# Kernel optimization log

Measured on AMD Instinct MI355X. Metric: run time of the kernel, lower is better.

Reference implementation:

```python
import jax, jax.numpy as jnp
import numpy as np

B, N, DIM = 4, 4096, 1024
HEADS, DIM_HEAD = 16, 64
HD = HEADS * DIM_HEAD  # 1024
SCALE = DIM_HEAD ** -0.5


def setup_inputs() -> dict:
    key = jax.random.key(0)
    k0, k1, k2 = jax.random.split(key, 3)
    x = jax.random.normal(k0, (B, N, DIM), dtype=jnp.float32)
    # nn.Linear(dim, 3*hd): weight stored transposed here as (dim, 3*hd) for x @ W
    Wqkv = jax.random.normal(k1, (DIM, 3 * HD), dtype=jnp.float32) * 0.02
    bqkv = jnp.zeros((3 * HD,), dtype=jnp.float32)
    Wout = jax.random.normal(k2, (HD, DIM), dtype=jnp.float32) * 0.02
    bout = jnp.zeros((DIM,), dtype=jnp.float32)
    return {"x": x, "Wqkv": Wqkv, "bqkv": bqkv, "Wout": Wout, "bout": bout}


def reference(x, Wqkv, bqkv, Wout, bout):
    b, n, _ = x.shape
    # qkv: (b, n, 3*hd) -> (b, n, 3, hd)
    qkv = (x @ Wqkv + bqkv).reshape(b, n, 3, HD)
    # permute(2,0,3,1) in torch: q,k,v each have shape (b, hd, n)
    # (NOTE: heads are NOT split out in the original module; attention runs over
    #  the feature axis. We reproduce that math exactly.)
    q = jnp.swapaxes(qkv[:, :, 0, :], 1, 2)  # (b, hd, n)
    k = jnp.swapaxes(qkv[:, :, 1, :], 1, 2)
    v = jnp.swapaxes(qkv[:, :, 2, :], 1, 2)
    # dots: (b, hd, hd)
    dots = jnp.einsum('bfn,bgn->bfg', q, k) * SCALE
    attn = jax.nn.softmax(dots, axis=-1)
    # out: (b, hd, n), then row-major reinterpret to (b, n, hd) as torch reshape does
    out = jnp.einsum('bfg,bgn->bfn', attn, v).reshape(b, n, HD)
    return out @ Wout + bout
```

## Files before the change

### kernel.cpp

```cpp
#include <hip/hip_runtime.h>
#include <hip/hip_bf16.h>

typedef _Float16 f16x8 __attribute__((ext_vector_type(8)));
typedef float f32x4 __attribute__((ext_vector_type(4)));
typedef unsigned short u16x4 __attribute__((ext_vector_type(4)));
typedef unsigned short u16x8 __attribute__((ext_vector_type(8)));

__device__ __forceinline__ unsigned short f2h(float f) {
    _Float16 h = (_Float16)f;
    union { _Float16 h; unsigned short u; } v; v.h = h;
    return v.u;
}

__device__ __forceinline__ void gload16(const void* g, void* s) {
    __builtin_amdgcn_global_load_lds((const __attribute__((address_space(1))) void*)g,
                                     (__attribute__((address_space(3))) void*)s, 16, 0, 0);
}

__global__ __launch_bounds__(256)
void zero_f32(float* __restrict__ p, int n4) {
    int i = blockIdx.x * 256 + threadIdx.x, st = gridDim.x * 256;
    for (; i < n4; i += st)
        reinterpret_cast<float4*>(p)[i] = make_float4(0.f, 0.f, 0.f, 0.f);
}

__global__ __launch_bounds__(256)
void cvt_f32_f16(const float* __restrict__ in, unsigned short* __restrict__ out, int n8) {
    int i = blockIdx.x * 256 + threadIdx.x, st = gridDim.x * 256;
    for (; i < n8; i += st) {
        float4 v0 = reinterpret_cast<const float4*>(in)[2 * i];
        float4 v1 = reinterpret_cast<const float4*>(in)[2 * i + 1];
        float a[8] = {v0.x, v0.y, v0.z, v0.w, v1.x, v1.y, v1.z, v1.w};
        u16x8 h;
        #pragma unroll
        for (int j = 0; j < 8; ++j) h[j] = f2h(a[j]);
        reinterpret_cast<u16x8*>(out)[i] = h;
    }
}

__global__ __launch_bounds__(256)
void transpose_cvt(const float* __restrict__ in, unsigned short* __restrict__ ot,
                   int R, int C) {
    __shared__ float T[64][65];
    const int r0 = blockIdx.y * 64, c0 = blockIdx.x * 64;
    const int t = threadIdx.x;
    const int lr = t >> 2, lcq = (t & 3) * 16;
    #pragma unroll
    for (int q = 0; q < 4; ++q) {
        float4 v = *reinterpret_cast<const float4*>(&in[(long long)(r0 + lr) * C + c0 + lcq + q * 4]);
        T[lr][lcq + q * 4 + 0] = v.x; T[lr][lcq + q * 4 + 1] = v.y;
        T[lr][lcq + q * 4 + 2] = v.z; T[lr][lcq + q * 4 + 3] = v.w;
    }
    __syncthreads();
    const int oc = t >> 2, orq = (t & 3) * 16;
    #pragma unroll
    for (int q = 0; q < 4; ++q) {
        u16x4 hv;
        #pragma unroll
        for (int j = 0; j < 4; ++j) hv[j] = f2h(T[orq + q * 4 + j][oc]);
        long long o = (long long)(c0 + oc) * R + r0 + orq + q * 4;
        *reinterpret_cast<u16x4*>(&ot[o]) = hv;
    }
}

template<int EPI>
__global__ __launch_bounds__(256)
void gemm_f16(const unsigned short* __restrict__ A, const unsigned short* __restrict__ B,
              int sk_shift, int ks_size,
              long long lda, long long ldb,
              long long sA, long long sB, long long sC,
              float* __restrict__ Cf, unsigned short* __restrict__ Ch, long long ldc,
              const float* __restrict__ bias, float scale,
              unsigned short* __restrict__ qt, unsigned short* __restrict__ kt,
              unsigned short* __restrict__ vout)
{
    __shared__ __align__(16) unsigned short SMEM[2][2][128][32];

    const int tid  = threadIdx.x;
    const int wave = tid >> 6, lane = tid & 63;
    const int m0 = blockIdx.y * 128, n0 = blockIdx.x * 128;
    const int bz = (int)(blockIdx.z >> sk_shift);
    const int ks = (int)(blockIdx.z & ((1u << sk_shift) - 1));
    const int kbeg = ks * ks_size, kend = kbeg + ks_size;
    const int wm = (wave >> 1) * 64, wn = (wave & 1) * 64;
    const int fr = lane & 15, kslot = lane >> 4;
    const int srow = lane >> 2;

    const unsigned short* Ag = A + sA * bz + (long long)m0 * lda;
    const unsigned short* Bg = B + sB * bz + (long long)n0 * ldb;
    char* const sBase0 = (char*)&SMEM[0][0][0][0];
    char* const sBase1 = (char*)&SMEM[1][0][0][0];

    f32x4 acc[4][4] = {};

    auto STAGE = [&](char* base, int k0) {
        #pragma unroll
        for (int i = 0; i < 2; ++i) {
            const int r = i * 64 + wave * 16 + srow;
            const int qsrc = ((lane & 3) ^ ((r >> 1) & 3)) * 8;
            gload16(Ag + (long long)r * lda + k0 + qsrc, base + i * 4096 + wave * 1024);
            gload16(Bg + (long long)r * ldb + k0 + qsrc, base + 8192 + i * 4096 + wave * 1024);
        }
    };

    STAGE(sBase0, kbeg);
    __syncthreads();

    int cur = 0;
    for (int k0 = kbeg; k0 < kend; k0 += 32) {
        char* const rd = cur ? sBase1 : sBase0;
        char* const wr = cur ? sBase0 : sBase1;
        if (k0 + 32 < kend) STAGE(wr, k0 + 32);

        f16x8 af[4], bf[4];
        #pragma unroll
        for (int t = 0; t < 4; ++t) {
            const int ra = wm + t * 16 + fr;
            const int rb = wn + t * 16 + fr;
            af[t] = *reinterpret_cast<const f16x8*>(rd + ra * 64 + ((kslot ^ ((ra >> 1) & 3)) << 4));
            bf[t] = *reinterpret_cast<const f16x8*>(rd + 8192 + rb * 64 + ((kslot ^ ((rb >> 1) & 3)) << 4));
        }
        __builtin_amdgcn_s_setprio(1);
        #pragma unroll
        for (int mi = 0; mi < 4; ++mi)
            #pragma unroll
            for (int ni = 0; ni < 4; ++ni)
                acc[mi][ni] = __builtin_amdgcn_mfma_f32_16x16x32_f16(af[mi], bf[ni], acc[mi][ni], 0, 0, 0);
        __builtin_amdgcn_s_setprio(0);
        __syncthreads();
        cur ^= 1;
    }

    unsigned short (*LT)[72] = reinterpret_cast<unsigned short(*)[72]>(sBase0 + wave * 2304);

    const int rb4 = (lane >> 4) * 4;

    if (EPI == 1 || EPI == 4) {
        #pragma unroll
        for (int mi = 0; mi < 4; ++mi) {
            const int rloc = wm + mi * 16 + rb4;
            #pragma unroll
            for (int ni = 0; ni < 4; ++ni) {
                const int c = n0 + wn + ni * 16 + fr;
                const float bv = (EPI == 1) ? bias[c] : 0.0f;
                long long base = sC * bz + (long long)(m0 + rloc) * ldc + c;
                #pragma unroll
                for (int rr = 0; rr < 4; ++rr) {
                    float v = acc[mi][ni][rr] * scale + bv;
                    if (EPI == 1) Cf[base + (long long)rr * ldc] = v;
                    else          atomicAdd(&Cf[base + (long long)rr * ldc], v);
                }
            }
        }
    } else if (EPI == 2) {
        #pragma unroll
        for (int mi = 0; mi < 4; ++mi) {
            #pragma unroll
            for (int ni = 0; ni < 4; ++ni)
                #pragma unroll
                for (int rr = 0; rr < 4; ++rr)
                    LT[rb4 + rr][ni * 16 + fr] = f2h(acc[mi][ni][rr] * scale);
            #pragma unroll
            for (int q = 0; q < 2; ++q) {
                const int r_l = q * 8 + (lane >> 3);
                const int f0  = (lane & 7) * 8;
                u16x8 hv = *reinterpret_cast<const u16x8*>(&LT[r_l][f0]);
                long long base = sC * bz + (long long)(m0 + wm + mi * 16 + r_l) * ldc + (n0 + wn) + f0;
                *reinterpret_cast<u16x8*>(&Ch[base]) = hv;
            }
        }
    } else {
        const int segw = (n0 + wn) >> 10;
        const int tokb = m0 + wm;
        const int bloc = tokb >> 12;
        const int nbb  = tokb & 4095;
        if (segw < 2) {
            unsigned short* pt = (segw == 0) ? qt : kt;
            #pragma unroll
            for (int ni = 0; ni < 4; ++ni) {
                const float bv = bias[n0 + wn + ni * 16 + fr];
                #pragma unroll
                for (int mi = 0; mi < 4; ++mi) {
                    u16x4 hv;
                    #pragma unroll
                    for (int rr = 0; rr < 4; ++rr)
                        hv[rr] = f2h(acc[mi][ni][rr] * scale + bv);
                    *reinterpret_cast<u16x4*>(&LT[fr][mi * 16 + rb4]) = hv;
                }
                #pragma unroll
                for (int q = 0; q < 4; ++q) {
                    const int f_l = q * 4 + (lane >> 4);
                    const int t0  = (lane & 15) * 4;
                    u16x4 hv = *reinterpret_cast<const u16x4*>(&LT[f_l][t0]);
                    const int lc = (n0 + wn + ni * 16 + f_l) & 1023;
                    *reinterpret_cast<u16x4*>(&pt[(long long)bloc * 4194304 +
                        (long long)lc * 4096 + nbb + t0]) = hv;
                }
            }
        } else {
            const int lc0 = (n0 + wn) & 1023;
            #pragma unroll
            for (int mi = 0; mi < 4; ++mi) {
                #pragma unroll
                for (int ni = 0; ni < 4; ++ni) {
                    const float bv = bias[n0 + wn + ni * 16 + fr];
                    #pragma unroll
                    for (int rr = 0; rr < 4; ++rr)
                        LT[rb4 + rr][ni * 16 + fr] = f2h(acc[mi][ni][rr] * scale + bv);
                }
                #pragma unroll
                for (int q = 0; q < 2; ++q) {
                    const int r_l = q * 8 + (lane >> 3);
                    const int f0  = (lane & 7) * 8;
                    u16x8 hv = *reinterpret_cast<const u16x8*>(&LT[r_l][f0]);
                    const int tok = nbb + mi * 16 + r_l;
                    *reinterpret_cast<u16x8*>(&vout[(long long)bloc * 4194304 +
                        (long long)tok * 1024 + lc0 + f0]) = hv;
                }
            }
        }
    }
}

__global__ __launch_bounds__(256)
void softmax_rows_1024(const float* __restrict__ in, unsigned short* __restrict__ out)
{
    const int tid = threadIdx.x;
    const int wave = tid >> 6, lane = tid & 63;
    const long long rowoff = (long long)blockIdx.x * 1024;
    float4 v = reinterpret_cast<const float4*>(in + rowoff)[tid];

    float mx = fmaxf(fmaxf(v.x, v.y), fmaxf(v.z, v.w));
    #pragma unroll
    for (int o = 32; o > 0; o >>= 1) mx = fmaxf(mx, __shfl_xor(mx, o));
    __shared__ float rmax[4];
    if (lane == 0) rmax[wave] = mx;
    __syncthreads();
    mx = fmaxf(fmaxf(rmax[0], rmax[1]), fmaxf(rmax[2], rmax[3]));

    float e0 = expf(v.x - mx), e1 = expf(v.y - mx), e2 = expf(v.z - mx), e3 = expf(v.w - mx);
    float s = e0 + e1 + e2 + e3;
    #pragma unroll
    for (int o = 32; o > 0; o >>= 1) s += __shfl_xor(s, o);
    __shared__ float rsum[4];
    if (lane == 0) rsum[wave] = s;
    __syncthreads();
    s = rsum[0] + rsum[1] + rsum[2] + rsum[3];
    float inv = 1.0f / s;

    u16x4 o4;
    o4[0] = f2h(e0 * inv); o4[1] = f2h(e1 * inv);
    o4[2] = f2h(e2 * inv); o4[3] = f2h(e3 * inv);
    *reinterpret_cast<u16x4*>(out + rowoff + tid * 4) = o4;
}

extern "C" void kernel_launch(void* const* d_in, const int* in_sizes, int n_in,
                              void* d_out, int out_size, void* d_ws, size_t ws_size,
                              hipStream_t stream)
{
    const float* x    = (const float*)d_in[0];
    const float* Wqkv = (const float*)d_in[1];
    const float* bqkv = (const float*)d_in[2];
    const float* Wout = (const float*)d_in[3];
    const float* bout = (const float*)d_in[4];
    float* out = (float*)d_out;

    char* ws = (char*)d_ws;
    unsigned short* xf   = (unsigned short*)(ws);
    unsigned short* Wq16 = (unsigned short*)(ws + 33554432);
    unsigned short* Wo16 = (unsigned short*)(ws + 39845888);
    unsigned short* Qt   = (unsigned short*)(ws + 41943040);
    unsigned short* Kt   = (unsigned short*)(ws + 75497472);
    unsigned short* V    = (unsigned short*)(ws + 109051904);
    float*          dots = (float*)(ws + 142606336);
    unsigned short* attn = (unsigned short*)(ws + 159383552);
    unsigned short* omid = (unsigned short*)(ws + 167772160);

    zero_f32<<<dim3(2048), dim3(256), 0, stream>>>(dots, 1048576);

    cvt_f32_f16<<<dim3(2048), dim3(256), 0, stream>>>(x, xf, 2097152);
    transpose_cvt<<<dim3(48, 16), dim3(256), 0, stream>>>(Wqkv, Wq16, 1024, 3072);
    transpose_cvt<<<dim3(16, 16), dim3(256), 0, stream>>>(Wout, Wo16, 1024, 1024);

    gemm_f16<3><<<dim3(24, 128, 1), dim3(256), 0, stream>>>(
        xf, Wq16, 0, 1024,
        1024LL, 1024LL, 0LL, 0LL, 0LL,
        nullptr, nullptr, 0LL, bqkv, 1.0f,
        Qt, Kt, V);

    gemm_f16<4><<<dim3(8, 8, 8), dim3(256), 0, stream>>>(
        Qt, Kt, 1, 2048,
        4096LL, 4096LL, 4194304LL, 4194304LL, 1048576LL,
        dots, nullptr, 1024LL, nullptr, 0.125f,
        nullptr, nullptr, nullptr);

    softmax_rows_1024<<<dim3(4096), dim3(256), 0, stream>>>(dots, attn);

    gemm_f16<2><<<dim3(32, 8, 4), dim3(256), 0, stream>>>(
        attn, V, 0, 1024,
        1024LL, 1024LL, 1048576LL, 4194304LL, 4194304LL,
        nullptr, omid, 4096LL, nullptr, 1.0f,
        nullptr, nullptr, nullptr);

    gemm_f16<1><<<dim3(8, 128, 1), dim3(256), 0, stream>>>(
        omid, Wo16, 0, 1024,
        1024LL, 1024LL, 0LL, 0LL, 0LL,
        out, nullptr, 1024LL, bout, 1.0f,
        nullptr, nullptr, nullptr);
}
```

Measured before the change: 336.5 us.

## Use triple-buffered LDS pipeline with partial vmcnt waits in GEMM

Moves the GEMM main loop from double buffering to a three-stage LDS ring, prefetching two k-tiles ahead. Full __syncthreads is replaced by an s_waitcnt vmcnt(4) that waits only for the oldest tile's loads, plus a raw s_barrier. This aims to hide global-load latency better, at the cost of 50% more LDS per block, which could lower occupancy. The hand-written waitcnt logic also relies on each STAGE issuing exactly four loads per thread.

```diff
diff --git a/kernel.cpp b/kernel.cpp
--- a/kernel.cpp
+++ b/kernel.cpp
@@ -74,22 +74,25 @@
               unsigned short* __restrict__ qt, unsigned short* __restrict__ kt,
               unsigned short* __restrict__ vout)
 {
-    __shared__ __align__(16) unsigned short SMEM[2][2][128][32];
+    __shared__ __align__(16) unsigned short SMEM[3][2][128][32];
 
     const int tid  = threadIdx.x;
     const int wave = tid >> 6, lane = tid & 63;
     const int m0 = blockIdx.y * 128, n0 = blockIdx.x * 128;
     const int bz = (int)(blockIdx.z >> sk_shift);
     const int ks = (int)(blockIdx.z & ((1u << sk_shift) - 1));
-    const int kbeg = ks * ks_size, kend = kbeg + ks_size;
+    const int kbeg = ks * ks_size;
+    const int nsteps = ks_size >> 5;
     const int wm = (wave >> 1) * 64, wn = (wave & 1) * 64;
     const int fr = lane & 15, kslot = lane >> 4;
     const int srow = lane >> 2;
 
     const unsigned short* Ag = A + sA * bz + (long long)m0 * lda;
     const unsigned short* Bg = B + sB * bz + (long long)n0 * ldb;
-    char* const sBase0 = (char*)&SMEM[0][0][0][0];
-    char* const sBase1 = (char*)&SMEM[1][0][0][0];
+    char* b0 = (char*)&SMEM[0][0][0][0];
+    char* b1 = (char*)&SMEM[1][0][0][0];
+    char* b2 = (char*)&SMEM[2][0][0][0];
+    char* const sBase0 = b0;
 
     f32x4 acc[4][4] = {};
 
@@ -103,22 +106,23 @@
         }
     };
 
-    STAGE(sBase0, kbeg);
-    __syncthreads();
-
-    int cur = 0;
-    for (int k0 = kbeg; k0 < kend; k0 += 32) {
-        char* const rd = cur ? sBase1 : sBase0;
-        char* const wr = cur ? sBase0 : sBase1;
-        if (k0 + 32 < kend) STAGE(wr, k0 + 32);
+    STAGE(b0, kbeg);
+    STAGE(b1, kbeg + 32);
+    asm volatile("s_waitcnt vmcnt(4)" ::: "memory");
+    __builtin_amdgcn_s_barrier();
+    __builtin_amdgcn_sched_barrier(0);
+
+    for (int t = 0; t < nsteps; ++t) {
+        const bool pf = (t + 2 < nsteps);
+        if (pf) STAGE(b2, kbeg + (t + 2) * 32);
 
         f16x8 af[4], bf[4];
         #pragma unroll
-        for (int t = 0; t < 4; ++t) {
-            const int ra = wm + t * 16 + fr;
-            const int rb = wn + t * 16 + fr;
-            af[t] = *reinterpret_cast<const f16x8*>(rd + ra * 64 + ((kslot ^ ((ra >> 1) & 3)) << 4));
-            bf[t] = *reinterpret_cast<const f16x8*>(rd + 8192 + rb * 64 + ((kslot ^ ((rb >> 1) & 3)) << 4));
+        for (int q = 0; q < 4; ++q) {
+            const int ra = wm + q * 16 + fr;
+            const int rb = wn + q * 16 + fr;
+            af[q] = *reinterpret_cast<const f16x8*>(b0 + ra * 64 + ((kslot ^ ((ra >> 1) & 3)) << 4));
+            bf[q] = *reinterpret_cast<const f16x8*>(b0 + 8192 + rb * 64 + ((kslot ^ ((rb >> 1) & 3)) << 4));
         }
         __builtin_amdgcn_s_setprio(1);
         #pragma unroll
@@ -127,9 +131,16 @@
             for (int ni = 0; ni < 4; ++ni)
                 acc[mi][ni] = __builtin_amdgcn_mfma_f32_16x16x32_f16(af[mi], bf[ni], acc[mi][ni], 0, 0, 0);
         __builtin_amdgcn_s_setprio(0);
-        __syncthreads();
-        cur ^= 1;
-    }
+
+        if (t + 1 < nsteps) {
+            if (pf) asm volatile("s_waitcnt vmcnt(4) lgkmcnt(0)" ::: "memory");
+            else    asm volatile("s_waitcnt vmcnt(0) lgkmcnt(0)" ::: "memory");
+            __builtin_amdgcn_s_barrier();
+            __builtin_amdgcn_sched_barrier(0);
+        }
+        char* tmp = b0; b0 = b1; b1 = b2; b2 = tmp;
+    }
+    __syncthreads();
 
     unsigned short (*LT)[72] = reinterpret_cast<unsigned short(*)[72]>(sBase0 + wave * 2304);
 
```

New measurement: 325.2 us. -3.4%, faster.
